# Kernel tuning notes

Measured on AMD Instinct MI355X. Metric: run time of the kernel, lower is better.

The kernel has to match this reference:

```python
import jax, jax.numpy as jnp
import numpy as np

N_NODES = 50000


def gcn_conv(x, W, b, src, dst, n_nodes):
    """PyG-style GCNConv: self-loops + symmetric deg^-1/2 normalization.

    x: [N, Fin], W: [Fin, Fout], b: [Fout], src/dst: [E] int.
    """
    h = x @ W  # [N, Fout] -- transform before aggregation (small GEMM)
    loop = jnp.arange(n_nodes, dtype=src.dtype)
    src2 = jnp.concatenate([src, loop])  # [E+N]
    dst2 = jnp.concatenate([dst, loop])
    # degree on target nodes (all edge weights = 1, includes self loops)
    deg = jax.ops.segment_sum(jnp.ones(src2.shape[0], dtype=h.dtype), dst2,
                              num_segments=n_nodes)
    dinv = jnp.where(deg > 0, jax.lax.rsqrt(deg), 0.0)
    norm = dinv[src2] * dinv[dst2]  # [E+N]
    msg = h[src2] * norm[:, None]   # gather + scale (memory bound)
    out = jax.ops.segment_sum(msg, dst2, num_segments=n_nodes)  # scatter-add
    return out + b


def setup_inputs() -> dict:
    key = jax.random.key(0)
    ks = jax.random.split(key, 8)
    input_dim, hidden_dim, output_dim = 128, 64, 64
    n_edges = 800000
    x = jax.random.normal(ks[0], (N_NODES, input_dim), dtype=jnp.float32)
    edge_index = jax.random.randint(ks[1], (2, n_edges), 0, N_NODES,
                                    dtype=jnp.int32)
    def glorot(k, fan_in, fan_out):
        s = jnp.sqrt(6.0 / (fan_in + fan_out)).astype(jnp.float32)
        return jax.random.uniform(k, (fan_in, fan_out), jnp.float32, -s, s)
    return {
        "x": x,
        "edge_index": edge_index,
        "W1": glorot(ks[2], input_dim, hidden_dim),
        "b1": jnp.zeros((hidden_dim,), jnp.float32),
        "W2": glorot(ks[3], hidden_dim, output_dim),
        "b2": jnp.zeros((output_dim,), jnp.float32),
        "Wfc": glorot(ks[4], output_dim, 1),
        "bfc": jnp.zeros((1,), jnp.float32),
    }


def reference(x, edge_index, W1, b1, W2, b2, Wfc, bfc):
    src, dst = edge_index[0], edge_index[1]
    h = gcn_conv(x, W1, b1, src, dst, N_NODES)
    h = jax.nn.relu(h)
    h = gcn_conv(h, W2, b2, src, dst, N_NODES)
    logits = h @ Wfc + bfc  # [N, 1]
    return jax.nn.sigmoid(logits)
```

## Files before the change

kernel.cpp:

```cpp
#include <hip/hip_runtime.h>
#include <hip/hip_bf16.h>

#define NN 50000
#define FIN 128
#define NT (NN / 16)
#define NREG 196
#define RCAP 5120
#define SLAB 8960

typedef unsigned short u16;
typedef unsigned int u32;
typedef __attribute__((ext_vector_type(8))) short short8;
typedef __attribute__((ext_vector_type(4))) float floatx4;

__device__ __forceinline__ float b2f(u16 v) {
  union { u32 u; float f; } x; x.u = ((u32)v) << 16; return x.f;
}
__device__ __forceinline__ u16 f2b(float f) {
  union { u32 u; float f; } x; x.f = f;
  u32 r = x.u + 0x7FFFu + ((x.u >> 16) & 1u);
  return (u16)(r >> 16);
}

__global__ __launch_bounds__(256) void k_prep_binA(
    const u32* __restrict__ xw, int nxw, const void* __restrict__ w1, int n1w,
    const void* __restrict__ w2, int n2w, const void* __restrict__ wf, int nfw,
    const u16* __restrict__ b2, const u16* __restrict__ bfc,
    u16* __restrict__ W1h, u16* __restrict__ W1l, float* __restrict__ w2f,
    float* __restrict__ cbias, int* __restrict__ flags,
    const int* __restrict__ src, const int* __restrict__ dst, int E,
    u32* __restrict__ bucket, int* __restrict__ gtail,
    u16* __restrict__ g, float* __restrict__ tvec) {
  int t = threadIdx.x;
  int blk = blockIdx.x;
  if (blk >= 33) {
    __shared__ int hist[NREG];
    __shared__ int base[NREG];
    for (int i = t; i < NREG; i += 256) hist[i] = 0;
    __syncthreads();
    int sl = blk - 33, nsl = 256;
    int lo = (int)((long long)sl * E / nsl);
    int hi = (int)((long long)(sl + 1) * E / nsl);
    for (int e = lo + t; e < hi; e += 256) atomicAdd(&hist[dst[e] >> 8], 1);
    __syncthreads();
    for (int i = t; i < NREG; i += 256) {
      int c = hist[i];
      base[i] = (c > 0) ? atomicAdd(&gtail[i], c) : 0;
      hist[i] = 0;
    }
    __syncthreads();
    for (int e = lo + t; e < hi; e += 256) {
      int d = dst[e];
      int r = d >> 8;
      int ofs = base[r] + atomicAdd(&hist[r], 1);
      if (ofs < RCAP)
        bucket[(size_t)r * RCAP + ofs] = ((u32)(d & 255) << 16) | (u32)src[e];
    }
    return;
  }
  __shared__ int sc[2];
  if (t < 2) sc[t] = 0;
  __syncthreads();
  if (blk < 32) {
    const u32* p = (const u32*)w1;
    int samples = n1w < 1024 ? n1w : 1024;
    int score = 0;
    for (int i = t; i < samples; i += 256) {
      u32 w = p[i];
      u32 e = (w >> 7) & 0xFFu;
      score += (e >= 100u && e <= 132u) ? 1 : -1;
    }
    if (score) atomicAdd(&sc[0], score);
    if (blk == 0) {
      int sn = nxw < 1024 ? nxw : 1024;
      int sx = 0;
      for (int i = t; i < sn; i += 256) {
        u32 w = xw[i];
        u32 e = (w >> 7) & 0xFFu;
        sx += (e >= 100u && e <= 132u) ? 1 : -1;
      }
      if (sx) atomicAdd(&sc[1], sx);
    }
    __syncthreads();
    int f1 = sc[0] > 0;
    if (blk == 0 && t == 0) {
      flags[0] = sc[1] > 0;
      flags[1] = f1;
    }
    int i = blk * 256 + t;
    int j = i & 7, L = (i >> 3) & 63, f = i >> 9;
    int k = (f >> 2) * 32 + (L >> 4) * 8 + j;
    int n = (f & 3) * 16 + (L & 15);
    int idx = k * 64 + n;
    float v = f1 ? b2f(((const u16*)w1)[idx]) : ((const float*)w1)[idx];
    u16 hb = f2b(v);
    W1h[i] = hb;
    W1l[i] = f2b(v - b2f(hb));
  } else {
    const u32* p2 = (const u32*)w2;
    const u32* pf = (const u32*)wf;
    int n2s = n2w < 1024 ? n2w : 1024;
    int nfs = nfw < 1024 ? nfw : 1024;
    int s2 = 0, sf = 0;
    for (int i = t; i < n2s; i += 256) {
      u32 w = p2[i];
      u32 e = (w >> 7) & 0xFFu;
      s2 += (e >= 100u && e <= 132u) ? 1 : -1;
    }
    for (int i = t; i < nfs; i += 256) {
      u32 w = pf[i];
      u32 e = (w >> 7) & 0xFFu;
      sf += (e >= 100u && e <= 132u) ? 1 : -1;
    }
    if (s2) atomicAdd(&sc[0], s2);
    if (sf) atomicAdd(&sc[1], sf);
    __syncthreads();
    int f2 = sc[0] > 0, f3 = sc[1] > 0;
    if (t == 0) { flags[2] = f2; flags[3] = f3; }
    if (t < 64) {
      float acc = 0.f;
      for (int j = 0; j < 64; ++j) {
        float w2v = f2 ? b2f(((const u16*)w2)[t * 64 + j])
                       : ((const float*)w2)[t * 64 + j];
        float wfv = f3 ? b2f(((const u16*)wf)[j]) : ((const float*)wf)[j];
        acc += w2v * wfv;
      }
      w2f[t] = acc;
    } else if (t == 64) {
      float acc = b2f(bfc[0]);
      for (int j = 0; j < 64; ++j) {
        float wfv = f3 ? b2f(((const u16*)wf)[j]) : ((const float*)wf)[j];
        acc += b2f(b2[j]) * wfv;
      }
      cbias[0] = acc;
    } else if (t >= 128 && t < 192) {
      g[(size_t)NN * 64 + (t - 128)] = 0;
    } else if (t == 192) {
      tvec[NN] = 0.f;
    }
  }
}

__global__ __launch_bounds__(256) void k_binB1(const u32* __restrict__ bucket,
                                               const int* __restrict__ gtail,
                                               int* __restrict__ cnt,
                                               int* __restrict__ rowstart,
                                               float* __restrict__ dinv) {
  __shared__ int h[256];
  __shared__ int smem[4];
  int r = blockIdx.x, t = threadIdx.x;
  h[t] = 0;
  __syncthreads();
  int n = gtail[r];
  if (n > RCAP) n = RCAP;
  const u32* b = bucket + (size_t)r * RCAP;
  for (int i = t; i < n; i += 256) atomicAdd(&h[b[i] >> 16], 1);
  __syncthreads();
  int v = r * 256 + t;
  int c = (v < NN) ? h[t] : 0;
  if (v < NN) {
    cnt[v] = c;
    dinv[v] = rsqrtf((float)(c + 1));
  }
  int p = (c + 15) & ~15;
  int lane = t & 63, w = t >> 6;
  int xv = p;
  for (int d = 1; d < 64; d <<= 1) {
    int y = __shfl_up(xv, d);
    if (lane >= d) xv += y;
  }
  if (lane == 63) smem[w] = xv;
  __syncthreads();
  int add = 0;
  for (int j = 0; j < w; ++j) add += smem[j];
  xv += add;
  if (v < NN) rowstart[v] = r * SLAB + xv - p;
}

__global__ __launch_bounds__(256) void k_gemm_scatter(
    const u32* __restrict__ bucket, const int* __restrict__ gtail,
    const int* __restrict__ rowstart, const int* __restrict__ cnt,
    u16* __restrict__ csr,
    const void* __restrict__ X, const u16* __restrict__ Wh,
    const u16* __restrict__ Wl, const float* __restrict__ dinv,
    u16* __restrict__ g, const int* __restrict__ flags) {
  int t = threadIdx.x;
  if (blockIdx.x < NREG) {
    __shared__ int off[256];
    int r = blockIdx.x;
    int v = r * 256 + t;
    int grs = (v < NN) ? rowstart[v] : 0;
    off[t] = grs;
    __syncthreads();
    int n = gtail[r];
    if (n > RCAP) n = RCAP;
    const u32* b = bucket + (size_t)r * RCAP;
    for (int i = t; i < n; i += 256) {
      u32 p = b[i];
      int pos = atomicAdd(&off[p >> 16], 1);
      csr[pos] = (u16)(p & 0xFFFFu);
    }
    __syncthreads();
    if (v < NN) {
      int end = grs + ((cnt[v] + 15) & ~15);
      for (int pos = off[t]; pos < end; ++pos) csr[pos] = (u16)NN;
    }
    return;
  }
  constexpr int KC = FIN / 32;
  int wave = t >> 6, lane = t & 63;
  int rt = (blockIdx.x - NREG) * 4 + wave;
  if (rt >= NT) return;
  int m = rt * 16 + (lane & 15);
  int q = (lane >> 4) * 8;
  bool xb = flags[0] != 0;

  short8 ah[KC], al[KC];
  if (xb) {
    const u16* xr = (const u16*)X + (size_t)m * FIN + q;
#pragma unroll
    for (int kc = 0; kc < KC; ++kc) ah[kc] = *(const short8*)(xr + kc * 32);
  } else {
    const float* xr = (const float*)X + (size_t)m * FIN + q;
#pragma unroll
    for (int kc = 0; kc < KC; ++kc) {
      float4 v0 = *(const float4*)(xr + kc * 32);
      float4 v1 = *(const float4*)(xr + kc * 32 + 4);
      float v[8] = {v0.x, v0.y, v0.z, v0.w, v1.x, v1.y, v1.z, v1.w};
      short8 h8, l8;
#pragma unroll
      for (int j = 0; j < 8; ++j) {
        u16 hb = f2b(v[j]);
        h8[j] = (short)hb;
        l8[j] = (short)f2b(v[j] - b2f(hb));
      }
      ah[kc] = h8;
      al[kc] = l8;
    }
  }

  int row0 = rt * 16 + (lane >> 4) * 4;
  int c0 = lane & 15;
  float dvr[4];
#pragma unroll
  for (int r = 0; r < 4; ++r) dvr[r] = dinv[row0 + r];
#pragma unroll
  for (int ct = 0; ct < 4; ++ct) {
    short8 bh[KC], bl[KC];
#pragma unroll
    for (int kc = 0; kc < KC; ++kc) {
      size_t fo = ((size_t)((kc * 4 + ct) * 64 + lane)) * 8;
      bh[kc] = *(const short8*)(Wh + fo);
      bl[kc] = *(const short8*)(Wl + fo);
    }
    floatx4 acc = (floatx4)(0.f);
#pragma unroll
    for (int kc = 0; kc < KC; ++kc) {
      if (!xb)
        acc = __builtin_amdgcn_mfma_f32_16x16x32_bf16(al[kc], bh[kc], acc, 0, 0, 0);
      acc = __builtin_amdgcn_mfma_f32_16x16x32_bf16(ah[kc], bl[kc], acc, 0, 0, 0);
      acc = __builtin_amdgcn_mfma_f32_16x16x32_bf16(ah[kc], bh[kc], acc, 0, 0, 0);
    }
    size_t o = (size_t)row0 * 64 + ct * 16 + c0;
#pragma unroll
    for (int r = 0; r < 4; ++r) g[o + (size_t)r * 64] = f2b(acc[r] * dvr[r]);
  }
}

__global__ __launch_bounds__(256) void k_agg1t(const u16* __restrict__ g,
                                               const float* __restrict__ dinv,
                                               const int* __restrict__ rowstart,
                                               const int* __restrict__ cnt,
                                               const u16* __restrict__ csr,
                                               const u16* __restrict__ bias,
                                               const float* __restrict__ w2f,
                                               float* __restrict__ tvec) {
  int tid = threadIdx.x;
  int wave = tid >> 6, lane = tid & 63;
  int v = (blockIdx.x * 4 + wave) * 4;
  int rs[4], pd[4];
  float dvl[4], acc[4];
  int pm = 0;
#pragma unroll
  for (int n = 0; n < 4; ++n) {
    rs[n] = rowstart[v + n];
    pd[n] = (cnt[v + n] + 15) & ~15;
    dvl[n] = dinv[v + n];
    acc[n] = b2f(g[(size_t)(v + n) * 64 + lane]);
    pm = pd[n] > pm ? pd[n] : pm;
  }
  for (int j = 0; j < pm; j += 16) {
    u32 cw[4][8];
    bool act[4];
#pragma unroll
    for (int n = 0; n < 4; ++n) {
      act[n] = j < pd[n];
      if (act[n]) {
        int b = rs[n] + j;
        uint4 c0 = *(const uint4*)(csr + b);
        uint4 c1 = *(const uint4*)(csr + b + 8);
        cw[n][0] = c0.x; cw[n][1] = c0.y; cw[n][2] = c0.z; cw[n][3] = c0.w;
        cw[n][4] = c1.x; cw[n][5] = c1.y; cw[n][6] = c1.z; cw[n][7] = c1.w;
      }
    }
    float hh[4][16];
#pragma unroll
    for (int n = 0; n < 4; ++n) {
      if (act[n]) {
#pragma unroll
        for (int i = 0; i < 8; ++i) {
          hh[n][2 * i] = b2f(g[(size_t)(cw[n][i] & 0xFFFFu) * 64 + lane]);
          hh[n][2 * i + 1] = b2f(g[(size_t)(cw[n][i] >> 16) * 64 + lane]);
        }
      }
    }
#pragma unroll
    for (int n = 0; n < 4; ++n) {
      if (act[n]) {
        float s0 = (hh[n][0] + hh[n][1]) + (hh[n][2] + hh[n][3]);
        float s1 = (hh[n][4] + hh[n][5]) + (hh[n][6] + hh[n][7]);
        float s2 = (hh[n][8] + hh[n][9]) + (hh[n][10] + hh[n][11]);
        float s3 = (hh[n][12] + hh[n][13]) + (hh[n][14] + hh[n][15]);
        acc[n] += (s0 + s1) + (s2 + s3);
      }
    }
  }
  float bv = b2f(bias[lane]);
  float wfv = w2f[lane];
  float val[4];
#pragma unroll
  for (int n = 0; n < 4; ++n) {
    val[n] = fmaxf(dvl[n] * acc[n] + bv, 0.0f) * wfv;
    for (int o = 32; o > 0; o >>= 1) val[n] += __shfl_xor(val[n], o);
  }
#pragma unroll
  for (int n = 0; n < 4; ++n)
    if (lane == n) tvec[v + n] = dvl[n] * val[n];
}

__global__ __launch_bounds__(256) void k_aggz(const float* __restrict__ tvec,
                                              const float* __restrict__ dinv,
                                              const int* __restrict__ rowstart,
                                              const int* __restrict__ cnt,
                                              const u16* __restrict__ csr,
                                              const float* __restrict__ cbias,
                                              void* __restrict__ out,
                                              const int* __restrict__ flags) {
  int tid = threadIdx.x;
  int wave = tid >> 6, lane = tid & 63;
  int sub = lane >> 4, slot = lane & 15;
  int v = blockIdx.x * 16 + wave * 4 + sub;
  int rs = rowstart[v];
  int pdeg = (cnt[v] + 15) & ~15;
  float acc = 0.f;
  for (int j = slot; j < pdeg; j += 16) acc += tvec[csr[rs + j]];
  for (int o = 8; o > 0; o >>= 1) acc += __shfl_xor(acc, o);
  if (slot == 0) {
    float dv = dinv[v];
    float z = dv * (acc + tvec[v]) + cbias[0];
    float sg = 1.0f / (1.0f + __expf(-z));
    if (flags[0]) ((u16*)out)[v] = f2b(sg);
    else ((float*)out)[v] = sg;
  }
}

extern "C" void kernel_launch(void* const* d_in, const int* in_sizes, int n_in,
                              void* d_out, int out_size, void* d_ws, size_t ws_size,
                              hipStream_t stream) {
  const void* x = d_in[0];
  const int* ei = (const int*)d_in[1];
  const void* W1 = d_in[2];
  const u16* b1 = (const u16*)d_in[3];
  const void* W2 = d_in[4];
  const u16* b2 = (const u16*)d_in[5];
  const void* Wfc = d_in[6];
  const u16* bfc = (const u16*)d_in[7];

  int E = in_sizes[1] / 2;
  const int* src = ei;
  const int* dst = ei + E;

  char* base = (char*)d_ws;
  size_t off = 0;
  auto alloc = [&](size_t bytes) {
    void* p = base + off;
    off = (off + bytes + 255) & ~(size_t)255;
    return p;
  };
  int* flags = (int*)alloc(8 * 4);
  u16* W1h = (u16*)alloc((size_t)FIN * 64 * 2);
  u16* W1l = (u16*)alloc((size_t)FIN * 64 * 2);
  float* w2f = (float*)alloc(64 * 4);
  float* cbias = (float*)alloc(4);
  int* cnt = (int*)alloc((size_t)NN * 4);
  int* rowstart = (int*)alloc((size_t)NN * 4);
  int* gtail = (int*)alloc((size_t)NREG * 4);
  u32* bucket = (u32*)alloc((size_t)NREG * RCAP * 4);
  u16* csr = (u16*)alloc((size_t)NREG * SLAB * 2);
  float* dinv = (float*)alloc((size_t)NN * 4);
  u16* g = (u16*)alloc((size_t)(NN + 1) * 64 * 2);
  float* tvec = (float*)alloc((size_t)(NN + 1) * 4);

  hipMemsetAsync(gtail, 0, (size_t)NREG * 4, stream);
  k_prep_binA<<<289, 256, 0, stream>>>(
      (const u32*)x, in_sizes[0] / 2, W1, in_sizes[2] / 2, W2, in_sizes[4] / 2,
      Wfc, in_sizes[6] / 2, b2, bfc, W1h, W1l, w2f, cbias, flags, src, dst, E,
      bucket, gtail, g, tvec);
  k_binB1<<<NREG, 256, 0, stream>>>(bucket, gtail, cnt, rowstart, dinv);
  k_gemm_scatter<<<NREG + (NT + 3) / 4, 256, 0, stream>>>(
      bucket, gtail, rowstart, cnt, csr, x, W1h, W1l, dinv, g, flags);
  k_agg1t<<<NN / 16, 256, 0, stream>>>(g, dinv, rowstart, cnt, csr, b1, w2f,
                                       tvec);
  k_aggz<<<NN / 16, 256, 0, stream>>>(tvec, dinv, rowstart, cnt, csr, cbias,
                                      d_out, flags);
}
```

Before: 158.3 us.

## Fuse GCN pipeline into one cooperative persistent kernel with grid syncs

Replaces the memset plus five kernel launches with a single cooperative kernel of 512 persistent blocks that uses grid.sync between phases. It also overlaps edge binning with the X·W1 GEMM in one phase, and moves the dinv row scaling of g into the CSR build phase instead of the GEMM epilogue. The aim is to remove launch gaps and inter-kernel drains. The cost is that later phases run with fewer blocks than before, each grid barrier has its own overhead, and if the cooperative launch fails it falls back to the old path.

```diff
diff --git a/kernel.cpp b/kernel.cpp
--- a/kernel.cpp
+++ b/kernel.cpp
@@ -1,12 +1,17 @@
 #include <hip/hip_runtime.h>
 #include <hip/hip_bf16.h>
+#include <hip/hip_cooperative_groups.h>
+
+namespace cg = cooperative_groups;
 
 #define NN 50000
 #define FIN 128
 #define NT (NN / 16)
+#define GB ((NT + 3) / 4)
 #define NREG 196
 #define RCAP 5120
 #define SLAB 8960
+#define NB 512
 
 typedef unsigned short u16;
 typedef unsigned int u32;
@@ -20,6 +25,330 @@
   union { u32 u; float f; } x; x.f = f;
   u32 r = x.u + 0x7FFFu + ((x.u >> 16) & 1u);
   return (u16)(r >> 16);
+}
+
+struct KArgs {
+  const u32* xw; const void* w1; const void* w2; const void* wf;
+  const u16* b1; const u16* b2; const u16* bfc;
+  const int* src; const int* dst;
+  u16* W1h; u16* W1l; float* w2f; float* cbias; int* flags;
+  u32* bucket; int* gtail; int* cnt; int* rowstart; float* dinv;
+  u16* csr; u16* g; float* tvec; void* out;
+  int nxw, n1w, n2w, nfw, E;
+};
+
+__device__ __forceinline__ int detect_score(const u32* p, int nw, int t) {
+  int samples = nw < 1024 ? nw : 1024;
+  int score = 0;
+  for (int i = t; i < samples; i += 256) {
+    u32 w = p[i];
+    u32 e = (w >> 7) & 0xFFu;
+    score += (e >= 100u && e <= 132u) ? 1 : -1;
+  }
+  return score;
+}
+
+__device__ __forceinline__ void gemm_tile(int rt, int lane, const KArgs& a,
+                                          bool xb) {
+  constexpr int KC = FIN / 32;
+  int m = rt * 16 + (lane & 15);
+  int q = (lane >> 4) * 8;
+  short8 ah[KC], al[KC];
+  if (xb) {
+    const u16* xr = (const u16*)a.xw + (size_t)m * FIN + q;
+#pragma unroll
+    for (int kc = 0; kc < KC; ++kc) ah[kc] = *(const short8*)(xr + kc * 32);
+  } else {
+    const float* xr = (const float*)a.xw + (size_t)m * FIN + q;
+#pragma unroll
+    for (int kc = 0; kc < KC; ++kc) {
+      float4 v0 = *(const float4*)(xr + kc * 32);
+      float4 v1 = *(const float4*)(xr + kc * 32 + 4);
+      float v[8] = {v0.x, v0.y, v0.z, v0.w, v1.x, v1.y, v1.z, v1.w};
+      short8 h8, l8;
+#pragma unroll
+      for (int j = 0; j < 8; ++j) {
+        u16 hb = f2b(v[j]);
+        h8[j] = (short)hb;
+        l8[j] = (short)f2b(v[j] - b2f(hb));
+      }
+      ah[kc] = h8;
+      al[kc] = l8;
+    }
+  }
+  int row0 = rt * 16 + (lane >> 4) * 4;
+  int c0 = lane & 15;
+#pragma unroll
+  for (int ct = 0; ct < 4; ++ct) {
+    short8 bh[KC], bl[KC];
+#pragma unroll
+    for (int kc = 0; kc < KC; ++kc) {
+      size_t fo = ((size_t)((kc * 4 + ct) * 64 + lane)) * 8;
+      bh[kc] = *(const short8*)(a.W1h + fo);
+      bl[kc] = *(const short8*)(a.W1l + fo);
+    }
+    floatx4 acc = (floatx4)(0.f);
+#pragma unroll
+    for (int kc = 0; kc < KC; ++kc) {
+      if (!xb)
+        acc = __builtin_amdgcn_mfma_f32_16x16x32_bf16(al[kc], bh[kc], acc, 0, 0, 0);
+      acc = __builtin_amdgcn_mfma_f32_16x16x32_bf16(ah[kc], bl[kc], acc, 0, 0, 0);
+      acc = __builtin_amdgcn_mfma_f32_16x16x32_bf16(ah[kc], bh[kc], acc, 0, 0, 0);
+    }
+    size_t o = (size_t)row0 * 64 + ct * 16 + c0;
+#pragma unroll
+    for (int r = 0; r < 4; ++r) a.g[o + (size_t)r * 64] = f2b(acc[r]);
+  }
+}
+
+__global__ __launch_bounds__(256, 2) void k_fused(KArgs a) {
+  cg::grid_group grid = cg::this_grid();
+  __shared__ int s_i[512];
+  __shared__ float s_f[256];
+  __shared__ int s_x[4];
+  int t = threadIdx.x;
+  int blk = blockIdx.x;
+  int lane = t & 63, wave = t >> 6;
+
+  if (blk < 32) {
+    if (t < 2) s_x[t] = 0;
+    __syncthreads();
+    int sc = detect_score((const u32*)a.w1, a.n1w, t);
+    if (sc) atomicAdd(&s_x[0], sc);
+    if (blk == 0) {
+      int sx = detect_score(a.xw, a.nxw, t);
+      if (sx) atomicAdd(&s_x[1], sx);
+    }
+    __syncthreads();
+    int f1 = s_x[0] > 0;
+    if (blk == 0 && t == 0) {
+      a.flags[0] = s_x[1] > 0;
+      a.flags[1] = f1;
+    }
+    int i = blk * 256 + t;
+    int j = i & 7, L = (i >> 3) & 63, f = i >> 9;
+    int k = (f >> 2) * 32 + (L >> 4) * 8 + j;
+    int n = (f & 3) * 16 + (L & 15);
+    int idx = k * 64 + n;
+    float v = f1 ? b2f(((const u16*)a.w1)[idx]) : ((const float*)a.w1)[idx];
+    u16 hb = f2b(v);
+    a.W1h[i] = hb;
+    a.W1l[i] = f2b(v - b2f(hb));
+  } else if (blk == 32) {
+    if (t < 2) s_x[t] = 0;
+    __syncthreads();
+    int s2 = detect_score((const u32*)a.w2, a.n2w, t);
+    int sf = detect_score((const u32*)a.wf, a.nfw, t);
+    if (s2) atomicAdd(&s_x[0], s2);
+    if (sf) atomicAdd(&s_x[1], sf);
+    for (int i = t; i < NREG; i += 256) a.gtail[i] = 0;
+    __syncthreads();
+    int f2 = s_x[0] > 0, f3 = s_x[1] > 0;
+    if (t == 0) { a.flags[2] = f2; a.flags[3] = f3; }
+    if (t < 64) {
+      float acc = 0.f;
+      for (int j = 0; j < 64; ++j) {
+        float w2v = f2 ? b2f(((const u16*)a.w2)[t * 64 + j])
+                       : ((const float*)a.w2)[t * 64 + j];
+        float wfv = f3 ? b2f(((const u16*)a.wf)[j]) : ((const float*)a.wf)[j];
+        acc += w2v * wfv;
+      }
+      a.w2f[t] = acc;
+    } else if (t == 64) {
+      float acc = b2f(a.bfc[0]);
+      for (int j = 0; j < 64; ++j) {
+        float wfv = f3 ? b2f(((const u16*)a.wf)[j]) : ((const float*)a.wf)[j];
+        acc += b2f(a.b2[j]) * wfv;
+      }
+      a.cbias[0] = acc;
+    } else if (t >= 128 && t < 192) {
+      a.g[(size_t)NN * 64 + (t - 128)] = 0;
+    } else if (t == 192) {
+      a.tvec[NN] = 0.f;
+    }
+  }
+  __threadfence();
+  grid.sync();
+
+  bool xb = a.flags[0] != 0;
+  for (int task = blk; task < 256 + GB; task += NB) {
+    if (task < 256) {
+      int* hist = s_i;
+      int* base = s_i + 256;
+      for (int i = t; i < NREG; i += 256) hist[i] = 0;
+      __syncthreads();
+      int lo = (int)((long long)task * a.E / 256);
+      int hi = (int)((long long)(task + 1) * a.E / 256);
+      for (int e = lo + t; e < hi; e += 256)
+        atomicAdd(&hist[a.dst[e] >> 8], 1);
+      __syncthreads();
+      for (int i = t; i < NREG; i += 256) {
+        int c = hist[i];
+        base[i] = (c > 0) ? atomicAdd(&a.gtail[i], c) : 0;
+        hist[i] = 0;
+      }
+      __syncthreads();
+      for (int e = lo + t; e < hi; e += 256) {
+        int d = a.dst[e];
+        int r = d >> 8;
+        int ofs = base[r] + atomicAdd(&hist[r], 1);
+        if (ofs < RCAP)
+          a.bucket[(size_t)r * RCAP + ofs] =
+              ((u32)(d & 255) << 16) | (u32)a.src[e];
+      }
+      __syncthreads();
+    } else {
+      int rt = (task - 256) * 4 + wave;
+      if (rt < NT) gemm_tile(rt, lane, a, xb);
+    }
+  }
+  __threadfence();
+  grid.sync();
+
+  if (blk < NREG) {
+    int* h = s_i;
+    int* off = s_i + 256;
+    h[t] = 0;
+    __syncthreads();
+    int n = a.gtail[blk];
+    if (n > RCAP) n = RCAP;
+    const u32* b = a.bucket + (size_t)blk * RCAP;
+    for (int i = t; i < n; i += 256) atomicAdd(&h[b[i] >> 16], 1);
+    __syncthreads();
+    int v = blk * 256 + t;
+    int c = (v < NN) ? h[t] : 0;
+    float dv = rsqrtf((float)(c + 1));
+    if (v < NN) {
+      a.cnt[v] = c;
+      a.dinv[v] = dv;
+    }
+    s_f[t] = dv;
+    int p = (c + 15) & ~15;
+    int xv = p;
+    for (int d = 1; d < 64; d <<= 1) {
+      int y = __shfl_up(xv, d);
+      if (lane >= d) xv += y;
+    }
+    if (lane == 63) s_x[wave] = xv;
+    __syncthreads();
+    int add = 0;
+    for (int j = 0; j < wave; ++j) add += s_x[j];
+    xv += add;
+    int grs = blk * SLAB + xv - p;
+    if (v < NN) a.rowstart[v] = grs;
+    off[t] = grs;
+    __syncthreads();
+    for (int i = t; i < n; i += 256) {
+      u32 pk = b[i];
+      int pos = atomicAdd(&off[pk >> 16], 1);
+      a.csr[pos] = (u16)(pk & 0xFFFFu);
+    }
+    __syncthreads();
+    if (v < NN) {
+      int end = grs + p;
+      for (int pos = off[t]; pos < end; ++pos) a.csr[pos] = (u16)NN;
+    }
+    for (int ch = t; ch < 2048; ch += 256) {
+      int vv = blk * 256 + (ch >> 3);
+      if (vv < NN) {
+        float dvv = s_f[ch >> 3];
+        u16* gp = a.g + (size_t)vv * 64 + (ch & 7) * 8;
+        short8 q = *(short8*)gp;
+#pragma unroll
+        for (int j = 0; j < 8; ++j)
+          q[j] = (short)f2b(b2f((u16)q[j]) * dvv);
+        *(short8*)gp = q;
+      }
+    }
+  }
+  __threadfence();
+  grid.sync();
+
+  {
+    float bv = b2f(a.b1[lane]);
+    float wfv = a.w2f[lane];
+    for (int task = blk; task < NT; task += NB) {
+      int v = task * 16 + wave * 4;
+      int rs[4], pd[4];
+      float dvl[4], acc[4];
+      int pm = 0;
+#pragma unroll
+      for (int n = 0; n < 4; ++n) {
+        rs[n] = a.rowstart[v + n];
+        pd[n] = (a.cnt[v + n] + 15) & ~15;
+        dvl[n] = a.dinv[v + n];
+        acc[n] = b2f(a.g[(size_t)(v + n) * 64 + lane]);
+        pm = pd[n] > pm ? pd[n] : pm;
+      }
+      for (int j = 0; j < pm; j += 16) {
+        u32 cw[4][8];
+        bool act[4];
+#pragma unroll
+        for (int n = 0; n < 4; ++n) {
+          act[n] = j < pd[n];
+          if (act[n]) {
+            int b = rs[n] + j;
+            uint4 c0 = *(const uint4*)(a.csr + b);
+            uint4 c1 = *(const uint4*)(a.csr + b + 8);
+            cw[n][0] = c0.x; cw[n][1] = c0.y; cw[n][2] = c0.z; cw[n][3] = c0.w;
+            cw[n][4] = c1.x; cw[n][5] = c1.y; cw[n][6] = c1.z; cw[n][7] = c1.w;
+          }
+        }
+        float hh[4][16];
+#pragma unroll
+        for (int n = 0; n < 4; ++n) {
+          if (act[n]) {
+#pragma unroll
+            for (int i = 0; i < 8; ++i) {
+              hh[n][2 * i] = b2f(a.g[(size_t)(cw[n][i] & 0xFFFFu) * 64 + lane]);
+              hh[n][2 * i + 1] = b2f(a.g[(size_t)(cw[n][i] >> 16) * 64 + lane]);
+            }
+          }
+        }
+#pragma unroll
+        for (int n = 0; n < 4; ++n) {
+          if (act[n]) {
+            float s0 = (hh[n][0] + hh[n][1]) + (hh[n][2] + hh[n][3]);
+            float s1 = (hh[n][4] + hh[n][5]) + (hh[n][6] + hh[n][7]);
+            float s2 = (hh[n][8] + hh[n][9]) + (hh[n][10] + hh[n][11]);
+            float s3 = (hh[n][12] + hh[n][13]) + (hh[n][14] + hh[n][15]);
+            acc[n] += (s0 + s1) + (s2 + s3);
+          }
+        }
+      }
+      float val[4];
+#pragma unroll
+      for (int n = 0; n < 4; ++n) {
+        val[n] = fmaxf(dvl[n] * acc[n] + bv, 0.0f) * wfv;
+        for (int o = 32; o > 0; o >>= 1) val[n] += __shfl_xor(val[n], o);
+      }
+#pragma unroll
+      for (int n = 0; n < 4; ++n)
+        if (lane == n) a.tvec[v + n] = dvl[n] * val[n];
+    }
+  }
+  __threadfence();
+  grid.sync();
+
+  {
+    int sub = lane >> 4, slot = lane & 15;
+    float cb = a.cbias[0];
+    for (int task = blk; task < NT; task += NB) {
+      int v = task * 16 + wave * 4 + sub;
+      int rs = a.rowstart[v];
+      int pdeg = (a.cnt[v] + 15) & ~15;
+      float acc = 0.f;
+      for (int j = slot; j < pdeg; j += 16) acc += a.tvec[a.csr[rs + j]];
+      for (int o = 8; o > 0; o >>= 1) acc += __shfl_xor(acc, o);
+      if (slot == 0) {
+        float dv = a.dinv[v];
+        float z = dv * (acc + a.tvec[v]) + cb;
+        float sg = 1.0f / (1.0f + __expf(-z));
+        if (xb) ((u16*)a.out)[v] = f2b(sg);
+        else ((float*)a.out)[v] = sg;
+      }
+    }
+  }
 }
 
 __global__ __launch_bounds__(256) void k_prep_binA(
@@ -38,9 +367,9 @@
     __shared__ int base[NREG];
     for (int i = t; i < NREG; i += 256) hist[i] = 0;
     __syncthreads();
-    int sl = blk - 33, nsl = 256;
-    int lo = (int)((long long)sl * E / nsl);
-    int hi = (int)((long long)(sl + 1) * E / nsl);
+    int sl = blk - 33;
+    int lo = (int)((long long)sl * E / 256);
+    int hi = (int)((long long)(sl + 1) * E / 256);
     for (int e = lo + t; e < hi; e += 256) atomicAdd(&hist[dst[e] >> 8], 1);
     __syncthreads();
     for (int i = t; i < NREG; i += 256) {
@@ -62,23 +391,10 @@
   if (t < 2) sc[t] = 0;
   __syncthreads();
   if (blk < 32) {
-    const u32* p = (const u32*)w1;
-    int samples = n1w < 1024 ? n1w : 1024;
-    int score = 0;
-    for (int i = t; i < samples; i += 256) {
-      u32 w = p[i];
-      u32 e = (w >> 7) & 0xFFu;
-      score += (e >= 100u && e <= 132u) ? 1 : -1;
-    }
+    int score = detect_score((const u32*)w1, n1w, t);
     if (score) atomicAdd(&sc[0], score);
     if (blk == 0) {
-      int sn = nxw < 1024 ? nxw : 1024;
-      int sx = 0;
-      for (int i = t; i < sn; i += 256) {
-        u32 w = xw[i];
-        u32 e = (w >> 7) & 0xFFu;
-        sx += (e >= 100u && e <= 132u) ? 1 : -1;
-      }
+      int sx = detect_score(xw, nxw, t);
       if (sx) atomicAdd(&sc[1], sx);
     }
     __syncthreads();
@@ -97,21 +413,8 @@
     W1h[i] = hb;
     W1l[i] = f2b(v - b2f(hb));
   } else {
-    const u32* p2 = (const u32*)w2;
-    const u32* pf = (const u32*)wf;
-    int n2s = n2w < 1024 ? n2w : 1024;
-    int nfs = nfw < 1024 ? nfw : 1024;
-    int s2 = 0, sf = 0;
-    for (int i = t; i < n2s; i += 256) {
-      u32 w = p2[i];
-      u32 e = (w >> 7) & 0xFFu;
-      s2 += (e >= 100u && e <= 132u) ? 1 : -1;
-    }
-    for (int i = t; i < nfs; i += 256) {
-      u32 w = pf[i];
-      u32 e = (w >> 7) & 0xFFu;
-      sf += (e >= 100u && e <= 132u) ? 1 : -1;
-    }
+    int s2 = detect_score((const u32*)w2, n2w, t);
+    int sf = detect_score((const u32*)wf, nfw, t);
     if (s2) atomicAdd(&sc[0], s2);
     if (sf) atomicAdd(&sc[1], sf);
     __syncthreads();
@@ -180,10 +483,10 @@
 __global__ __launch_bounds__(256) void k_gemm_scatter(
     const u32* __restrict__ bucket, const int* __restrict__ gtail,
     const int* __restrict__ rowstart, const int* __restrict__ cnt,
-    u16* __restrict__ csr,
-    const void* __restrict__ X, const u16* __restrict__ Wh,
-    const u16* __restrict__ Wl, const float* __restrict__ dinv,
-    u16* __restrict__ g, const int* __restrict__ flags) {
+    u16* __restrict__ csr, const void* __restrict__ X,
+    const u16* __restrict__ Wh, const u16* __restrict__ Wl,
+    const float* __restrict__ dinv, u16* __restrict__ g,
+    const int* __restrict__ flags) {
   int t = threadIdx.x;
   if (blockIdx.x < NREG) {
     __shared__ int off[256];
@@ -214,7 +517,6 @@
   int m = rt * 16 + (lane & 15);
   int q = (lane >> 4) * 8;
   bool xb = flags[0] != 0;
-
   short8 ah[KC], al[KC];
   if (xb) {
     const u16* xr = (const u16*)X + (size_t)m * FIN + q;
@@ -238,7 +540,6 @@
       al[kc] = l8;
     }
   }
-
   int row0 = rt * 16 + (lane >> 4) * 4;
   int c0 = lane & 15;
   float dvr[4];
@@ -401,16 +702,32 @@
   u16* g = (u16*)alloc((size_t)(NN + 1) * 64 * 2);
   float* tvec = (float*)alloc((size_t)(NN + 1) * 4);
 
-  hipMemsetAsync(gtail, 0, (size_t)NREG * 4, stream);
-  k_prep_binA<<<289, 256, 0, stream>>>(
-      (const u32*)x, in_sizes[0] / 2, W1, in_sizes[2] / 2, W2, in_sizes[4] / 2,
-      Wfc, in_sizes[6] / 2, b2, bfc, W1h, W1l, w2f, cbias, flags, src, dst, E,
-      bucket, gtail, g, tvec);
-  k_binB1<<<NREG, 256, 0, stream>>>(bucket, gtail, cnt, rowstart, dinv);
-  k_gemm_scatter<<<NREG + (NT + 3) / 4, 256, 0, stream>>>(
-      bucket, gtail, rowstart, cnt, csr, x, W1h, W1l, dinv, g, flags);
-  k_agg1t<<<NN / 16, 256, 0, stream>>>(g, dinv, rowstart, cnt, csr, b1, w2f,
-                                       tvec);
-  k_aggz<<<NN / 16, 256, 0, stream>>>(tvec, dinv, rowstart, cnt, csr, cbias,
-                                      d_out, flags);
-}
+  KArgs args;
+  args.xw = (const u32*)x; args.w1 = W1; args.w2 = W2; args.wf = Wfc;
+  args.b1 = b1; args.b2 = b2; args.bfc = bfc;
+  args.src = src; args.dst = dst;
+  args.W1h = W1h; args.W1l = W1l; args.w2f = w2f; args.cbias = cbias;
+  args.flags = flags; args.bucket = bucket; args.gtail = gtail;
+  args.cnt = cnt; args.rowstart = rowstart; args.dinv = dinv;
+  args.csr = csr; args.g = g; args.tvec = tvec; args.out = d_out;
+  args.nxw = in_sizes[0] / 2; args.n1w = in_sizes[2] / 2;
+  args.n2w = in_sizes[4] / 2; args.nfw = in_sizes[6] / 2; args.E = E;
+
+  void* kp[] = { &args };
+  hipError_t err = hipLaunchCooperativeKernel((void*)k_fused, dim3(NB),
+                                              dim3(256), kp, 0, stream);
+  if (err != hipSuccess) {
+    hipMemsetAsync(gtail, 0, (size_t)NREG * 4, stream);
+    k_prep_binA<<<289, 256, 0, stream>>>(
+        (const u32*)x, in_sizes[0] / 2, W1, in_sizes[2] / 2, W2,
+        in_sizes[4] / 2, Wfc, in_sizes[6] / 2, b2, bfc, W1h, W1l, w2f, cbias,
+        flags, src, dst, E, bucket, gtail, g, tvec);
+    k_binB1<<<NREG, 256, 0, stream>>>(bucket, gtail, cnt, rowstart, dinv);
+    k_gemm_scatter<<<NREG + GB, 256, 0, stream>>>(
+        bucket, gtail, rowstart, cnt, csr, x, W1h, W1l, dinv, g, flags);
+    k_agg1t<<<NN / 16, 256, 0, stream>>>(g, dinv, rowstart, cnt, csr, b1, w2f,
+                                         tvec);
+    k_aggz<<<NN / 16, 256, 0, stream>>>(tvec, dinv, rowstart, cnt, csr, cbias,
+                                        d_out, flags);
+  }
+}
```

Result: slower. 615.8 us (+289.1%).
